# Kernel tuning notes

Hardware: AMD Instinct MI355X
Metric: run time of the kernel (lower is better)

Reference implementation:

```python
import jax, jax.numpy as jnp
import numpy as np
from jax import lax

K = 7            # neighborhood kernel size (odd)
HEADS = 6
DIM = 96
HID = int(DIM * 2.66)   # 255, Restormer-style hidden width


def _ln(x, w, b):
    # WithBias_LayerNorm over the channel axis (to_3d makes C the last dim)
    mu = x.mean(axis=1, keepdims=True)
    var = x.var(axis=1, keepdims=True)  # biased, matches unbiased=False
    return (x - mu) / jnp.sqrt(var + 1e-5) * w[None, :, None, None] + b[None, :, None, None]


def _conv1x1(x, w, b=None):
    y = jnp.einsum('bchw,oc->bohw', x, w)
    return y if b is None else y + b[None, :, None, None]


def _dwconv3x3(x, w, b=None):
    y = lax.conv_general_dilated(x, w, (1, 1), 'SAME',
                                 feature_group_count=x.shape[1],
                                 dimension_numbers=('NCHW', 'OIHW', 'NCHW'))
    return y if b is None else y + b[None, :, None, None]


def _l2norm(x):
    n = jnp.sqrt(jnp.sum(x * x, axis=-1, keepdims=True))
    return x / jnp.maximum(n, 1e-12)  # F.normalize semantics


def _na(x, qkv_w, qkv_b, qkv_dw_w, qkv_dw_b, rpb, temperature, proj_w, proj_b):
    # NeighborhoodAttention with edge-clamped K x K windows and RPB (dilation=1)
    B, C, H, W = x.shape
    hd = C // HEADS
    qkv = _dwconv3x3(_conv1x1(x, qkv_w, qkv_b), qkv_dw_w, qkv_dw_b)      # [B,3C,H,W]
    qkv = qkv.reshape(B, 3, HEADS, hd, H, W).transpose(1, 0, 2, 4, 5, 3)  # [3,B,h,H,W,d]
    q, k, v = _l2norm(qkv[0]), _l2norm(qkv[1]), qkv[2]
    off = K // 2
    ii = jnp.arange(H)
    jj = jnp.arange(W)
    ri = jnp.clip(ii - off, 0, H - K)[:, None] + jnp.arange(K)   # [H,K] neighbor rows
    cj = jnp.clip(jj - off, 0, W - K)[:, None] + jnp.arange(K)   # [W,K] neighbor cols
    bi = ii[:, None] - ri + (K - 1)   # rpb row idx in [0, 2K-2]
    bj = jj[:, None] - cj + (K - 1)
    RI = jnp.repeat(ri.T, K, axis=0)  # [K*K,H]; offset o=ki*K+kj -> ri[:,ki]
    CI = jnp.tile(cj.T, (K, 1))       # [K*K,W]; offset o        -> cj[:,kj]

    def qk_body(_, rc):
        r, c = rc
        kk = k[:, :, r][:, :, :, c]                       # [B,h,H,W,d] gathered keys
        return None, jnp.einsum('bhijd,bhijd->bhij', q, kk)

    _, scores = lax.scan(qk_body, None, (RI, CI))          # [K*K,B,h,H,W]
    attn = jnp.moveaxis(scores, 0, -1)                     # [B,h,H,W,K*K]
    bias = rpb[:, bi][..., bj]                             # [h,H,K,W,K]
    bias = bias.transpose(0, 1, 3, 2, 4).reshape(HEADS, H, W, K * K)
    attn = (attn + bias[None]) * temperature[None, :, None, None, None]
    attn = jax.nn.softmax(attn, axis=-1)

    def av_body(acc, inp):
        r, c, a = inp
        vv = v[:, :, r][:, :, :, c]                        # [B,h,H,W,d] gathered values
        return acc + a[..., None] * vv, None

    out, _ = lax.scan(av_body, jnp.zeros_like(v), (RI, CI, jnp.moveaxis(attn, -1, 0)))
    out = out.transpose(0, 1, 4, 2, 3).reshape(B, C, H, W)
    return _conv1x1(out, proj_w, proj_b)


def _ffn(x, pin_w, dw_w, pout_w):
    y = _dwconv3x3(_conv1x1(x, pin_w), dw_w)               # [B,2*HID,H,W]
    x1, x2 = jnp.split(y, 2, axis=1)
    return _conv1x1(jax.nn.gelu(x1, approximate=False) * x2, pout_w)


def setup_inputs():
    key = jax.random.key(0)
    ks = jax.random.split(key, 18)
    def rn(k, shape, s=0.05):
        return jax.random.normal(k, shape, jnp.float32) * s
    return {
        'x': jax.random.normal(ks[0], (4, DIM, 128, 128), jnp.float32),
        'ln1_w': 1.0 + rn(ks[1], (DIM,), 0.02), 'ln1_b': rn(ks[2], (DIM,), 0.02),
        'qkv_w': rn(ks[3], (3 * DIM, DIM)), 'qkv_b': rn(ks[4], (3 * DIM,), 0.01),
        'qkv_dw_w': rn(ks[5], (3 * DIM, 1, 3, 3)), 'qkv_dw_b': rn(ks[6], (3 * DIM,), 0.01),
        'rpb': rn(ks[7], (HEADS, 2 * K - 1, 2 * K - 1), 0.02),
        'temperature': jnp.ones((HEADS,), jnp.float32),
        'proj_w': rn(ks[8], (DIM, DIM)), 'proj_b': rn(ks[9], (DIM,), 0.01),
        'ln2_w': 1.0 + rn(ks[10], (DIM,), 0.02), 'ln2_b': rn(ks[11], (DIM,), 0.02),
        'pin_w': rn(ks[12], (2 * HID, DIM)),
        'dw_w': rn(ks[13], (2 * HID, 1, 3, 3)),
        'pout_w': rn(ks[14], (DIM, HID)),
        'beta': rn(ks[15], (DIM,), 0.1), 'gamma': rn(ks[16], (DIM,), 0.1),
    }


def reference(x, ln1_w, ln1_b, qkv_w, qkv_b, qkv_dw_w, qkv_dw_b, rpb, temperature,
              proj_w, proj_b, ln2_w, ln2_b, pin_w, dw_w, pout_w, beta, gamma):
    x = x + _na(_ln(x, ln1_w, ln1_b), qkv_w, qkv_b, qkv_dw_w, qkv_dw_b,
                rpb, temperature, proj_w, proj_b) * beta[None, :, None, None]
    x = x + _ffn(_ln(x, ln2_w, ln2_b), pin_w, dw_w, pout_w) * gamma[None, :, None, None]
    return x
```

## Files before the change

### kernel.cpp

```cpp
#include <hip/hip_runtime.h>
#include <math.h>

#define HT   128
#define WD   128
#define HW   16384
#define NB_B 4
#define BHW  65536
#define CD   96
#define C3   288
#define NH   6
#define HD   16
#define HID  255
#define HID2 510
#define KK   7
#define NNB  49

__global__ __launch_bounds__(256) void prep_weights(
    const float* __restrict__ qkv_w, const float* __restrict__ qkv_b,
    const float* __restrict__ ln1_w, const float* __restrict__ ln1_b,
    const float* __restrict__ pin_w, const float* __restrict__ ln2_w,
    const float* __restrict__ ln2_b,
    const float* __restrict__ proj_w, const float* __restrict__ pout_w,
    float* __restrict__ w1t, float* __restrict__ s1, float* __restrict__ b1,
    float* __restrict__ w2t, float* __restrict__ s2, float* __restrict__ b2,
    float* __restrict__ wpt, float* __restrict__ wot)
{
    int o = blockIdx.x * 256 + threadIdx.x;
    if (o < C3) {
        float s = 0.f, bb = qkv_b[o];
        for (int c = 0; c < CD; ++c) {
            float wv = qkv_w[o*CD+c] * ln1_w[c];
            w1t[(size_t)c * C3 + o] = wv;
            s += wv;
            bb += qkv_w[o*CD+c] * ln1_b[c];
        }
        s1[o] = s; b1[o] = bb;
    }
    if (o < HID2) {
        float s = 0.f, bb = 0.f;
        for (int c = 0; c < CD; ++c) {
            float wv = pin_w[o*CD+c] * ln2_w[c];
            w2t[(size_t)c * 512 + o] = wv;
            s += wv;
            bb += pin_w[o*CD+c] * ln2_b[c];
        }
        s2[o] = s; b2[o] = bb;
    } else if (o < 512) {
        for (int c = 0; c < CD; ++c) w2t[(size_t)c * 512 + o] = 0.f;
        s2[o] = 0.f; b2[o] = 0.f;
    }
    if (o < CD) {
        for (int c = 0; c < CD; ++c)
            wpt[(size_t)c * CD + o] = proj_w[o*CD + c];
        for (int c = 0; c < HID; ++c)
            wot[(size_t)c * CD + o] = pout_w[o*HID + c];
    }
}

__global__ __launch_bounds__(256) void ln_stats(
    const float* __restrict__ x, float* __restrict__ mu, float* __restrict__ rsig)
{
    int t  = blockIdx.x * 256 + threadIdx.x;
    int p4 = t * 4;
    int b = p4 >> 14, p = p4 & (HW - 1);
    const float* xp = x + (size_t)b * CD * HW + p;
    float4 s = {0.f,0.f,0.f,0.f}, s2 = {0.f,0.f,0.f,0.f};
    #pragma unroll 4
    for (int c = 0; c < CD; ++c) {
        float4 v = *(const float4*)(xp + (size_t)c * HW);
        s.x += v.x; s.y += v.y; s.z += v.z; s.w += v.w;
        s2.x = fmaf(v.x, v.x, s2.x); s2.y = fmaf(v.y, v.y, s2.y);
        s2.z = fmaf(v.z, v.z, s2.z); s2.w = fmaf(v.w, v.w, s2.w);
    }
    const float inv = 1.f / CD;
    float4 m, r;
    m.x = s.x*inv; m.y = s.y*inv; m.z = s.z*inv; m.w = s.w*inv;
    r.x = rsqrtf(s2.x*inv - m.x*m.x + 1e-5f);
    r.y = rsqrtf(s2.y*inv - m.y*m.y + 1e-5f);
    r.z = rsqrtf(s2.z*inv - m.z*m.z + 1e-5f);
    r.w = rsqrtf(s2.w*inv - m.w*m.w + 1e-5f);
    *(float4*)(mu + p4)   = m;
    *(float4*)(rsig + p4) = r;
}

template<int EPI>
__global__ __launch_bounds__(256) void conv1x1(
    const float* __restrict__ in, const float* __restrict__ wT,
    int Cin, int Cout, int OS,
    const float* __restrict__ S, const float* __restrict__ Bb,
    const float* __restrict__ mu, const float* __restrict__ rsig,
    const float* __restrict__ res, const float* __restrict__ scale,
    float* __restrict__ out)
{
    int t  = blockIdx.y * 256 + threadIdx.x;
    int p4 = t * 4;
    int o0 = blockIdx.x * 16;
    int b = p4 >> 14, p = p4 & (HW - 1);
    const float* ip = in + (size_t)b * Cin * HW + p;
    float4 acc[16];
    #pragma unroll
    for (int u = 0; u < 16; ++u) acc[u] = {0.f,0.f,0.f,0.f};
    #pragma unroll 2
    for (int c = 0; c < Cin; ++c) {
        float4 v = *(const float4*)(ip + (size_t)c * HW);
        const float* wr = wT + (size_t)c * OS + o0;
        #pragma unroll
        for (int u = 0; u < 16; ++u) {
            float wv = wr[u];
            acc[u].x = fmaf(v.x, wv, acc[u].x);
            acc[u].y = fmaf(v.y, wv, acc[u].y);
            acc[u].z = fmaf(v.z, wv, acc[u].z);
            acc[u].w = fmaf(v.w, wv, acc[u].w);
        }
    }
    size_t obase = (size_t)b * Cout * HW + p;
    if (EPI == 0) {
        float4 m = *(const float4*)(mu + p4);
        float4 r = *(const float4*)(rsig + p4);
        #pragma unroll
        for (int u = 0; u < 16; ++u) {
            int o = o0 + u;
            if (o < Cout) {
                float so = S[o], bo = Bb[o];
                float4 ov;
                ov.x = r.x * (acc[u].x - m.x * so) + bo;
                ov.y = r.y * (acc[u].y - m.y * so) + bo;
                ov.z = r.z * (acc[u].z - m.z * so) + bo;
                ov.w = r.w * (acc[u].w - m.w * so) + bo;
                *(float4*)(out + obase + (size_t)o * HW) = ov;
            }
        }
    } else if (EPI == 1) {
        #pragma unroll
        for (int u = 0; u < 16; ++u) {
            int o = o0 + u;
            float bo = Bb[o], sc = scale[o];
            float4 rv = *(const float4*)(res + obase + (size_t)o * HW);
            float4 ov;
            ov.x = rv.x + (acc[u].x + bo) * sc;
            ov.y = rv.y + (acc[u].y + bo) * sc;
            ov.z = rv.z + (acc[u].z + bo) * sc;
            ov.w = rv.w + (acc[u].w + bo) * sc;
            *(float4*)(out + obase + (size_t)o * HW) = ov;
        }
    } else {
        #pragma unroll
        for (int u = 0; u < 16; ++u) {
            int o = o0 + u;
            float sc = scale[o];
            float4 rv = *(const float4*)(res + obase + (size_t)o * HW);
            float4 ov;
            ov.x = rv.x + acc[u].x * sc;
            ov.y = rv.y + acc[u].y * sc;
            ov.z = rv.z + acc[u].z * sc;
            ov.w = rv.w + acc[u].w * sc;
            *(float4*)(out + obase + (size_t)o * HW) = ov;
        }
    }
}

__global__ __launch_bounds__(256) void dwconv3x3(
    const float* __restrict__ in, const float* __restrict__ dwv,
    const float* __restrict__ bias, float* __restrict__ out, int Ch)
{
    int t  = blockIdx.x * 256 + threadIdx.x;
    int p4 = t * 4;
    int bc = blockIdx.y;
    int c  = bc % Ch;
    int h = p4 >> 7, wx = p4 & (WD - 1);
    const float* ip = in + (size_t)bc * HW;
    const float* wk = dwv + c * 9;
    float bz = bias[c];
    float a0 = bz, a1 = bz, a2 = bz, a3 = bz;
    #pragma unroll
    for (int ky = 0; ky < 3; ++ky) {
        int hh = h + ky - 1;
        if (hh < 0 || hh >= HT) continue;
        const float* rowp = ip + hh * WD + wx;
        float vm = (wx > 0)        ? rowp[-1] : 0.f;
        float4 v = *(const float4*)rowp;
        float vp = (wx + 4 < WD)   ? rowp[4]  : 0.f;
        float w0 = wk[ky*3+0], w1 = wk[ky*3+1], w2 = wk[ky*3+2];
        a0 = fmaf(vm,  w0, a0); a0 = fmaf(v.x, w1, a0); a0 = fmaf(v.y, w2, a0);
        a1 = fmaf(v.x, w0, a1); a1 = fmaf(v.y, w1, a1); a1 = fmaf(v.z, w2, a1);
        a2 = fmaf(v.y, w0, a2); a2 = fmaf(v.z, w1, a2); a2 = fmaf(v.w, w2, a2);
        a3 = fmaf(v.z, w0, a3); a3 = fmaf(v.w, w1, a3); a3 = fmaf(vp,  w2, a3);
    }
    float4 ov; ov.x = a0; ov.y = a1; ov.z = a2; ov.w = a3;
    *(float4*)(out + (size_t)bc * HW + p4) = ov;
}

__global__ __launch_bounds__(256) void dw_gate(
    const float* __restrict__ in, const float* __restrict__ dwv,
    float* __restrict__ out)
{
    int t  = blockIdx.x * 256 + threadIdx.x;
    int p4 = t * 4;
    int bj = blockIdx.y;
    int b = bj / HID, j = bj % HID;
    int h = p4 >> 7, wx = p4 & (WD - 1);
    const float* i1 = in + ((size_t)b * HID2 + j) * HW;
    const float* i2 = i1 + (size_t)HID * HW;
    const float* wk1 = dwv + j * 9;
    const float* wk2 = dwv + (j + HID) * 9;
    float a0=0.f,a1=0.f,a2=0.f,a3=0.f, g0=0.f,g1=0.f,g2=0.f,g3=0.f;
    #pragma unroll
    for (int ky = 0; ky < 3; ++ky) {
        int hh = h + ky - 1;
        if (hh < 0 || hh >= HT) continue;
        const float* r1 = i1 + hh * WD + wx;
        const float* r2 = i2 + hh * WD + wx;
        bool lm = (wx > 0), rp = (wx + 4 < WD);
        float um = lm ? r1[-1] : 0.f;
        float4 u = *(const float4*)r1;
        float up = rp ? r1[4] : 0.f;
        float vm = lm ? r2[-1] : 0.f;
        float4 v = *(const float4*)r2;
        float vp = rp ? r2[4] : 0.f;
        float w10 = wk1[ky*3+0], w11 = wk1[ky*3+1], w12 = wk1[ky*3+2];
        float w20 = wk2[ky*3+0], w21 = wk2[ky*3+1], w22 = wk2[ky*3+2];
        a0 = fmaf(um,  w10, a0); a0 = fmaf(u.x, w11, a0); a0 = fmaf(u.y, w12, a0);
        a1 = fmaf(u.x, w10, a1); a1 = fmaf(u.y, w11, a1); a1 = fmaf(u.z, w12, a1);
        a2 = fmaf(u.y, w10, a2); a2 = fmaf(u.z, w11, a2); a2 = fmaf(u.w, w12, a2);
        a3 = fmaf(u.z, w10, a3); a3 = fmaf(u.w, w11, a3); a3 = fmaf(up,  w12, a3);
        g0 = fmaf(vm,  w20, g0); g0 = fmaf(v.x, w21, g0); g0 = fmaf(v.y, w22, g0);
        g1 = fmaf(v.x, w20, g1); g1 = fmaf(v.y, w21, g1); g1 = fmaf(v.z, w22, g1);
        g2 = fmaf(v.y, w20, g2); g2 = fmaf(v.z, w21, g2); g2 = fmaf(v.w, w22, g2);
        g3 = fmaf(v.z, w20, g3); g3 = fmaf(v.w, w21, g3); g3 = fmaf(vp,  w22, g3);
    }
    const float is2 = 0.70710678118654752f;
    float4 ov;
    ov.x = 0.5f * a0 * (1.f + erff(a0 * is2)) * g0;
    ov.y = 0.5f * a1 * (1.f + erff(a1 * is2)) * g1;
    ov.z = 0.5f * a2 * (1.f + erff(a2 * is2)) * g2;
    ov.w = 0.5f * a3 * (1.f + erff(a3 * is2)) * g3;
    *(float4*)(out + ((size_t)b * HID + j) * HW + p4) = ov;
}

__global__ __launch_bounds__(256) void knorm(
    const float* __restrict__ qkv, float* __restrict__ rk)
{
    int t = blockIdx.x * 256 + threadIdx.x;
    int e = t * 4;
    int b = e / (NH * HW);
    int rem = e - b * (NH * HW);
    int h = rem / HW, p = rem & (HW - 1);
    const float* kp = qkv + ((size_t)b * C3 + CD + h * HD) * HW + p;
    float4 s = {0.f,0.f,0.f,0.f};
    #pragma unroll
    for (int d = 0; d < HD; ++d) {
        float4 v = *(const float4*)(kp + (size_t)d * HW);
        s.x = fmaf(v.x, v.x, s.x); s.y = fmaf(v.y, v.y, s.y);
        s.z = fmaf(v.z, v.z, s.z); s.w = fmaf(v.w, v.w, s.w);
    }
    float4 ov;
    ov.x = 1.f / fmaxf(sqrtf(s.x), 1e-12f);
    ov.y = 1.f / fmaxf(sqrtf(s.y), 1e-12f);
    ov.z = 1.f / fmaxf(sqrtf(s.z), 1e-12f);
    ov.w = 1.f / fmaxf(sqrtf(s.w), 1e-12f);
    *(float4*)(rk + e) = ov;
}

__global__ __launch_bounds__(256) void natten(
    const float* __restrict__ qkv, const float* __restrict__ rknorm,
    const float* __restrict__ rpb, const float* __restrict__ temp,
    float* __restrict__ out)
{
    __shared__ float srpb[169];
    int bh = blockIdx.z;
    int b = bh / NH, head = bh % NH;
    if (threadIdx.x < 169) srpb[threadIdx.x] = rpb[head * 169 + threadIdx.x];
    __syncthreads();

    int i = blockIdx.y * 16 + (threadIdx.x >> 4);
    int j = blockIdx.x * 16 + (threadIdx.x & 15);
    const float* qp = qkv + ((size_t)b * C3 + head * HD) * HW + i * WD + j;
    const float* kp = qkv + ((size_t)b * C3 + CD   + head * HD) * HW;
    const float* vp = qkv + ((size_t)b * C3 + 2*CD + head * HD) * HW;
    const float* rkp = rknorm + ((size_t)b * NH + head) * HW;
    float T = temp[head];

    float q[HD]; float qn = 0.f;
    #pragma unroll
    for (int d = 0; d < HD; ++d) { q[d] = qp[(size_t)d * HW]; qn = fmaf(q[d], q[d], qn); }
    qn = 1.f / fmaxf(sqrtf(qn), 1e-12f);
    #pragma unroll
    for (int d = 0; d < HD; ++d) q[d] *= qn;

    int ri0 = min(max(i - 3, 0), HT - KK);
    int cj0 = min(max(j - 3, 0), WD - KK);
    int bi0 = i - ri0 + 6;
    int bj0 = j - cj0 + 6;

    float s[NNB]; float m = -1e30f;
    #pragma unroll
    for (int o = 0; o < NNB; ++o) {
        int r = ri0 + o / KK, c = cj0 + o % KK;
        const float* kk = kp + r * WD + c;
        float dot = 0.f;
        #pragma unroll
        for (int d = 0; d < HD; ++d)
            dot = fmaf(q[d], kk[(size_t)d * HW], dot);
        float sv = (dot * rkp[r * WD + c]
                    + srpb[(bi0 - o / KK) * 13 + (bj0 - o % KK)]) * T;
        s[o] = sv;
        m = fmaxf(m, sv);
    }
    float l = 0.f;
    #pragma unroll
    for (int o = 0; o < NNB; ++o) { float pv = __expf(s[o] - m); s[o] = pv; l += pv; }
    float inv = 1.f / l;
    float ov[HD];
    #pragma unroll
    for (int d = 0; d < HD; ++d) ov[d] = 0.f;
    #pragma unroll
    for (int o = 0; o < NNB; ++o) {
        int r = ri0 + o / KK, c = cj0 + o % KK;
        const float* vv = vp + r * WD + c;
        float pv = s[o];
        #pragma unroll
        for (int d = 0; d < HD; ++d) ov[d] = fmaf(pv, vv[(size_t)d * HW], ov[d]);
    }
    float* op = out + ((size_t)b * CD + head * HD) * HW + i * WD + j;
    #pragma unroll
    for (int d = 0; d < HD; ++d) op[(size_t)d * HW] = ov[d] * inv;
}

extern "C" void kernel_launch(void* const* d_in, const int* in_sizes, int n_in,
                              void* d_out, int out_size, void* d_ws, size_t ws_size,
                              hipStream_t stream)
{
    const float* x        = (const float*)d_in[0];
    const float* ln1_w    = (const float*)d_in[1];
    const float* ln1_b    = (const float*)d_in[2];
    const float* qkv_w    = (const float*)d_in[3];
    const float* qkv_b    = (const float*)d_in[4];
    const float* qkv_dw_w = (const float*)d_in[5];
    const float* qkv_dw_b = (const float*)d_in[6];
    const float* rpb      = (const float*)d_in[7];
    const float* temp     = (const float*)d_in[8];
    const float* proj_w   = (const float*)d_in[9];
    const float* proj_b   = (const float*)d_in[10];
    const float* ln2_w    = (const float*)d_in[11];
    const float* ln2_b    = (const float*)d_in[12];
    const float* pin_w    = (const float*)d_in[13];
    const float* dw_w     = (const float*)d_in[14];
    const float* pout_w   = (const float*)d_in[15];
    const float* beta     = (const float*)d_in[16];
    const float* gamma    = (const float*)d_in[17];
    float* out = (float*)d_out;
    float* f   = (float*)d_ws;
    (void)in_sizes; (void)n_in; (void)out_size; (void)ws_size;

    float* W1T = f;
    float* W2T = W1T + 27648;
    float* WPT = W2T + 49152;
    float* WOT = WPT + 9216;
    float* S1  = WOT + 24480;
    float* B1  = S1 + 512;
    float* S2  = B1 + 512;
    float* B2  = S2 + 512;
    float* MU  = B2 + 512;
    float* RS  = MU + 65536;
    float* R1  = f + 262144;
    float* R2  = R1 + 18874368;
    float* R3  = R2 + 18874368;
    float* R4  = R3 + 16711680;
    float* RK  = R1;

    prep_weights<<<dim3(2), dim3(256), 0, stream>>>(
        qkv_w, qkv_b, ln1_w, ln1_b, pin_w, ln2_w, ln2_b, proj_w, pout_w,
        W1T, S1, B1, W2T, S2, B2, WPT, WOT);
    ln_stats<<<dim3(64), dim3(256), 0, stream>>>(x, MU, RS);
    conv1x1<0><<<dim3(18, 64), dim3(256), 0, stream>>>(
        x, W1T, CD, C3, C3, S1, B1, MU, RS, nullptr, nullptr, R1);
    dwconv3x3<<<dim3(16, NB_B * C3), dim3(256), 0, stream>>>(
        R1, qkv_dw_w, qkv_dw_b, R2, C3);
    knorm<<<dim3(384), dim3(256), 0, stream>>>(R2, RK);
    natten<<<dim3(8, 8, NB_B * NH), dim3(256), 0, stream>>>(R2, RK, rpb, temp, R3);
    conv1x1<1><<<dim3(6, 64), dim3(256), 0, stream>>>(
        R3, WPT, CD, CD, CD, nullptr, proj_b, nullptr, nullptr, x, beta, R4);
    ln_stats<<<dim3(64), dim3(256), 0, stream>>>(R4, MU, RS);
    conv1x1<0><<<dim3(32, 64), dim3(256), 0, stream>>>(
        R4, W2T, CD, HID2, 512, S2, B2, MU, RS, nullptr, nullptr, R1);
    dw_gate<<<dim3(16, NB_B * HID), dim3(256), 0, stream>>>(R1, dw_w, R3);
    conv1x1<2><<<dim3(6, 64), dim3(256), 0, stream>>>(
        R3, WOT, HID, CD, CD, nullptr, nullptr, nullptr, nullptr, R4, gamma, out);
}
```

Measured before the change: 592.0 us.

## Store K and V pixel-major with fused K normalization for neighborhood attention

Splits the depthwise conv into a Q kernel that keeps the channel-planar layout and K/V kernels that write a pixel-major [bh, HW, 16] layout, with K L2-normalized inside the conv. This drops the separate knorm pass. The attention kernel now reads each neighbor's 16-dim key and value as four float4 loads instead of 16 strided scalar loads, and temperature is folded into q and the bias table. The cost is that the K/V conv kernels hold 16 float4 accumulators per thread (more register pressure) and write with a 64-float stride between adjacent threads.

New measurement: 650.8 us. +9.9%, slower.

```diff
diff --git a/kernel.cpp b/kernel.cpp
--- a/kernel.cpp
+++ b/kernel.cpp
@@ -159,16 +159,16 @@
     }
 }
 
-__global__ __launch_bounds__(256) void dwconv3x3(
+__global__ __launch_bounds__(256) void dwconv_q(
     const float* __restrict__ in, const float* __restrict__ dwv,
-    const float* __restrict__ bias, float* __restrict__ out, int Ch)
+    const float* __restrict__ bias, float* __restrict__ out)
 {
     int t  = blockIdx.x * 256 + threadIdx.x;
     int p4 = t * 4;
     int bc = blockIdx.y;
-    int c  = bc % Ch;
+    int b = bc / CD, c = bc % CD;
     int h = p4 >> 7, wx = p4 & (WD - 1);
-    const float* ip = in + (size_t)bc * HW;
+    const float* ip = in + ((size_t)b * C3 + c) * HW;
     const float* wk = dwv + c * 9;
     float bz = bias[c];
     float a0 = bz, a1 = bz, a2 = bz, a3 = bz;
@@ -177,9 +177,9 @@
         int hh = h + ky - 1;
         if (hh < 0 || hh >= HT) continue;
         const float* rowp = ip + hh * WD + wx;
-        float vm = (wx > 0)        ? rowp[-1] : 0.f;
+        float vm = (wx > 0)      ? rowp[-1] : 0.f;
         float4 v = *(const float4*)rowp;
-        float vp = (wx + 4 < WD)   ? rowp[4]  : 0.f;
+        float vp = (wx + 4 < WD) ? rowp[4]  : 0.f;
         float w0 = wk[ky*3+0], w1 = wk[ky*3+1], w2 = wk[ky*3+2];
         a0 = fmaf(vm,  w0, a0); a0 = fmaf(v.x, w1, a0); a0 = fmaf(v.y, w2, a0);
         a1 = fmaf(v.x, w0, a1); a1 = fmaf(v.y, w1, a1); a1 = fmaf(v.z, w2, a1);
@@ -187,7 +187,75 @@
         a3 = fmaf(v.z, w0, a3); a3 = fmaf(v.w, w1, a3); a3 = fmaf(vp,  w2, a3);
     }
     float4 ov; ov.x = a0; ov.y = a1; ov.z = a2; ov.w = a3;
-    *(float4*)(out + (size_t)bc * HW + p4) = ov;
+    *(float4*)(out + ((size_t)b * CD + c) * HW + p4) = ov;
+}
+
+template<bool NORM>
+__global__ __launch_bounds__(256) void dwconv_t(
+    const float* __restrict__ in, const float* __restrict__ dwv,
+    const float* __restrict__ bias, float* __restrict__ outt, int cbase)
+{
+    int t  = blockIdx.x * 256 + threadIdx.x;
+    int p4 = t * 4;
+    int bh = blockIdx.y;
+    int b = bh / NH, head = bh % NH;
+    int h = p4 >> 7, wx = p4 & (WD - 1);
+    float4 acc[16];
+    #pragma unroll
+    for (int hd = 0; hd < 16; ++hd) {
+        int c = cbase + head * HD + hd;
+        const float* ip = in + ((size_t)b * C3 + c) * HW;
+        const float* wk = dwv + c * 9;
+        float bz = bias[c];
+        float a0 = bz, a1 = bz, a2 = bz, a3 = bz;
+        #pragma unroll
+        for (int ky = 0; ky < 3; ++ky) {
+            int hh = h + ky - 1;
+            if (hh < 0 || hh >= HT) continue;
+            const float* rowp = ip + hh * WD + wx;
+            float vm = (wx > 0)      ? rowp[-1] : 0.f;
+            float4 v = *(const float4*)rowp;
+            float vp = (wx + 4 < WD) ? rowp[4]  : 0.f;
+            float w0 = wk[ky*3+0], w1 = wk[ky*3+1], w2 = wk[ky*3+2];
+            a0 = fmaf(vm,  w0, a0); a0 = fmaf(v.x, w1, a0); a0 = fmaf(v.y, w2, a0);
+            a1 = fmaf(v.x, w0, a1); a1 = fmaf(v.y, w1, a1); a1 = fmaf(v.z, w2, a1);
+            a2 = fmaf(v.y, w0, a2); a2 = fmaf(v.z, w1, a2); a2 = fmaf(v.w, w2, a2);
+            a3 = fmaf(v.z, w0, a3); a3 = fmaf(v.w, w1, a3); a3 = fmaf(vp,  w2, a3);
+        }
+        acc[hd] = {a0, a1, a2, a3};
+    }
+    if (NORM) {
+        float n0=0.f, n1=0.f, n2=0.f, n3=0.f;
+        #pragma unroll
+        for (int hd = 0; hd < 16; ++hd) {
+            n0 = fmaf(acc[hd].x, acc[hd].x, n0);
+            n1 = fmaf(acc[hd].y, acc[hd].y, n1);
+            n2 = fmaf(acc[hd].z, acc[hd].z, n2);
+            n3 = fmaf(acc[hd].w, acc[hd].w, n3);
+        }
+        n0 = 1.f / fmaxf(sqrtf(n0), 1e-12f);
+        n1 = 1.f / fmaxf(sqrtf(n1), 1e-12f);
+        n2 = 1.f / fmaxf(sqrtf(n2), 1e-12f);
+        n3 = 1.f / fmaxf(sqrtf(n3), 1e-12f);
+        #pragma unroll
+        for (int hd = 0; hd < 16; ++hd) {
+            acc[hd].x *= n0; acc[hd].y *= n1; acc[hd].z *= n2; acc[hd].w *= n3;
+        }
+    }
+    float* op = outt + ((size_t)bh * HW + p4) * 16;
+#define STORE_PX(pi, comp)                                                    \
+    {                                                                         \
+        float4 w0 = {acc[ 0].comp, acc[ 1].comp, acc[ 2].comp, acc[ 3].comp}; \
+        float4 w1 = {acc[ 4].comp, acc[ 5].comp, acc[ 6].comp, acc[ 7].comp}; \
+        float4 w2 = {acc[ 8].comp, acc[ 9].comp, acc[10].comp, acc[11].comp}; \
+        float4 w3 = {acc[12].comp, acc[13].comp, acc[14].comp, acc[15].comp}; \
+        *(float4*)(op + pi*16 +  0) = w0;                                     \
+        *(float4*)(op + pi*16 +  4) = w1;                                     \
+        *(float4*)(op + pi*16 +  8) = w2;                                     \
+        *(float4*)(op + pi*16 + 12) = w3;                                     \
+    }
+    STORE_PX(0, x) STORE_PX(1, y) STORE_PX(2, z) STORE_PX(3, w)
+#undef STORE_PX
 }
 
 __global__ __launch_bounds__(256) void dw_gate(
@@ -237,53 +305,28 @@
     *(float4*)(out + ((size_t)b * HID + j) * HW + p4) = ov;
 }
 
-__global__ __launch_bounds__(256) void knorm(
-    const float* __restrict__ qkv, float* __restrict__ rk)
-{
-    int t = blockIdx.x * 256 + threadIdx.x;
-    int e = t * 4;
-    int b = e / (NH * HW);
-    int rem = e - b * (NH * HW);
-    int h = rem / HW, p = rem & (HW - 1);
-    const float* kp = qkv + ((size_t)b * C3 + CD + h * HD) * HW + p;
-    float4 s = {0.f,0.f,0.f,0.f};
-    #pragma unroll
-    for (int d = 0; d < HD; ++d) {
-        float4 v = *(const float4*)(kp + (size_t)d * HW);
-        s.x = fmaf(v.x, v.x, s.x); s.y = fmaf(v.y, v.y, s.y);
-        s.z = fmaf(v.z, v.z, s.z); s.w = fmaf(v.w, v.w, s.w);
-    }
-    float4 ov;
-    ov.x = 1.f / fmaxf(sqrtf(s.x), 1e-12f);
-    ov.y = 1.f / fmaxf(sqrtf(s.y), 1e-12f);
-    ov.z = 1.f / fmaxf(sqrtf(s.z), 1e-12f);
-    ov.w = 1.f / fmaxf(sqrtf(s.w), 1e-12f);
-    *(float4*)(rk + e) = ov;
-}
-
 __global__ __launch_bounds__(256) void natten(
-    const float* __restrict__ qkv, const float* __restrict__ rknorm,
-    const float* __restrict__ rpb, const float* __restrict__ temp,
-    float* __restrict__ out)
+    const float* __restrict__ qd, const float* __restrict__ kt,
+    const float* __restrict__ vt, const float* __restrict__ rpb,
+    const float* __restrict__ temp, float* __restrict__ out)
 {
     __shared__ float srpb[169];
     int bh = blockIdx.z;
     int b = bh / NH, head = bh % NH;
-    if (threadIdx.x < 169) srpb[threadIdx.x] = rpb[head * 169 + threadIdx.x];
+    float T = temp[head];
+    if (threadIdx.x < 169) srpb[threadIdx.x] = rpb[head * 169 + threadIdx.x] * T;
     __syncthreads();
 
     int i = blockIdx.y * 16 + (threadIdx.x >> 4);
     int j = blockIdx.x * 16 + (threadIdx.x & 15);
-    const float* qp = qkv + ((size_t)b * C3 + head * HD) * HW + i * WD + j;
-    const float* kp = qkv + ((size_t)b * C3 + CD   + head * HD) * HW;
-    const float* vp = qkv + ((size_t)b * C3 + 2*CD + head * HD) * HW;
-    const float* rkp = rknorm + ((size_t)b * NH + head) * HW;
-    float T = temp[head];
+    const float* qp  = qd + ((size_t)b * CD + head * HD) * HW + i * WD + j;
+    const float* ktb = kt + (size_t)bh * HW * 16;
+    const float* vtb = vt + (size_t)bh * HW * 16;
 
     float q[HD]; float qn = 0.f;
     #pragma unroll
     for (int d = 0; d < HD; ++d) { q[d] = qp[(size_t)d * HW]; qn = fmaf(q[d], q[d], qn); }
-    qn = 1.f / fmaxf(sqrtf(qn), 1e-12f);
+    qn = T / fmaxf(sqrtf(qn), 1e-12f);
     #pragma unroll
     for (int d = 0; d < HD; ++d) q[d] *= qn;
 
@@ -296,13 +339,14 @@
     #pragma unroll
     for (int o = 0; o < NNB; ++o) {
         int r = ri0 + o / KK, c = cj0 + o % KK;
-        const float* kk = kp + r * WD + c;
-        float dot = 0.f;
-        #pragma unroll
-        for (int d = 0; d < HD; ++d)
-            dot = fmaf(q[d], kk[(size_t)d * HW], dot);
-        float sv = (dot * rkp[r * WD + c]
-                    + srpb[(bi0 - o / KK) * 13 + (bj0 - o % KK)]) * T;
+        const float4* kk = (const float4*)(ktb + ((size_t)(r * WD + c)) * 16);
+        float4 k0 = kk[0], k1 = kk[1], k2 = kk[2], k3 = kk[3];
+        float d0 = q[0]*k0.x + q[1]*k0.y + q[2]*k0.z + q[3]*k0.w;
+        float d1 = q[4]*k1.x + q[5]*k1.y + q[6]*k1.z + q[7]*k1.w;
+        float d2 = q[8]*k2.x + q[9]*k2.y + q[10]*k2.z + q[11]*k2.w;
+        float d3 = q[12]*k3.x + q[13]*k3.y + q[14]*k3.z + q[15]*k3.w;
+        float sv = (d0 + d1) + (d2 + d3)
+                 + srpb[(bi0 - o / KK) * 13 + (bj0 - o % KK)];
         s[o] = sv;
         m = fmaxf(m, sv);
     }
@@ -316,10 +360,17 @@
     #pragma unroll
     for (int o = 0; o < NNB; ++o) {
         int r = ri0 + o / KK, c = cj0 + o % KK;
-        const float* vv = vp + r * WD + c;
+        const float4* vv = (const float4*)(vtb + ((size_t)(r * WD + c)) * 16);
+        float4 v0 = vv[0], v1 = vv[1], v2 = vv[2], v3 = vv[3];
         float pv = s[o];
-        #pragma unroll
-        for (int d = 0; d < HD; ++d) ov[d] = fmaf(pv, vv[(size_t)d * HW], ov[d]);
+        ov[0]  = fmaf(pv, v0.x, ov[0]);  ov[1]  = fmaf(pv, v0.y, ov[1]);
+        ov[2]  = fmaf(pv, v0.z, ov[2]);  ov[3]  = fmaf(pv, v0.w, ov[3]);
+        ov[4]  = fmaf(pv, v1.x, ov[4]);  ov[5]  = fmaf(pv, v1.y, ov[5]);
+        ov[6]  = fmaf(pv, v1.z, ov[6]);  ov[7]  = fmaf(pv, v1.w, ov[7]);
+        ov[8]  = fmaf(pv, v2.x, ov[8]);  ov[9]  = fmaf(pv, v2.y, ov[9]);
+        ov[10] = fmaf(pv, v2.z, ov[10]); ov[11] = fmaf(pv, v2.w, ov[11]);
+        ov[12] = fmaf(pv, v3.x, ov[12]); ov[13] = fmaf(pv, v3.y, ov[13]);
+        ov[14] = fmaf(pv, v3.z, ov[14]); ov[15] = fmaf(pv, v3.w, ov[15]);
     }
     float* op = out + ((size_t)b * CD + head * HD) * HW + i * WD + j;
     #pragma unroll
@@ -362,28 +413,34 @@
     float* B2  = S2 + 512;
     float* MU  = B2 + 512;
     float* RS  = MU + 65536;
-    float* R1  = f + 262144;
-    float* R2  = R1 + 18874368;
-    float* R3  = R2 + 18874368;
-    float* R4  = R3 + 16711680;
-    float* RK  = R1;
+    float* A   = f + 262144;
+    float* QKV = A;
+    float* QD  = A + 18874368;
+    float* KT  = QD + 6291456;
+    float* VT  = KT + 6291456;
+    float* AO  = A + 37748736;
+    float* X2  = A + 54460416;
 
     prep_weights<<<dim3(2), dim3(256), 0, stream>>>(
         qkv_w, qkv_b, ln1_w, ln1_b, pin_w, ln2_w, ln2_b, proj_w, pout_w,
         W1T, S1, B1, W2T, S2, B2, WPT, WOT);
     ln_stats<<<dim3(64), dim3(256), 0, stream>>>(x, MU, RS);
     conv1x1<0><<<dim3(18, 64), dim3(256), 0, stream>>>(
-        x, W1T, CD, C3, C3, S1, B1, MU, RS, nullptr, nullptr, R1);
-    dwconv3x3<<<dim3(16, NB_B * C3), dim3(256), 0, stream>>>(
-        R1, qkv_dw_w, qkv_dw_b, R2, C3);
-    knorm<<<dim3(384), dim3(256), 0, stream>>>(R2, RK);
-    natten<<<dim3(8, 8, NB_B * NH), dim3(256), 0, stream>>>(R2, RK, rpb, temp, R3);
+        x, W1T, CD, C3, C3, S1, B1, MU, RS, nullptr, nullptr, QKV);
+    dwconv_q<<<dim3(16, NB_B * CD), dim3(256), 0, stream>>>(
+        QKV, qkv_dw_w, qkv_dw_b, QD);
+    dwconv_t<true><<<dim3(16, NB_B * NH), dim3(256), 0, stream>>>(
+        QKV, qkv_dw_w, qkv_dw_b, KT, CD);
+    dwconv_t<false><<<dim3(16, NB_B * NH), dim3(256), 0, stream>>>(
+        QKV, qkv_dw_w, qkv_dw_b, VT, 2 * CD);
+    natten<<<dim3(8, 8, NB_B * NH), dim3(256), 0, stream>>>(
+        QD, KT, VT, rpb, temp, AO);
     conv1x1<1><<<dim3(6, 64), dim3(256), 0, stream>>>(
-        R3, WPT, CD, CD, CD, nullptr, proj_b, nullptr, nullptr, x, beta, R4);
-    ln_stats<<<dim3(64), dim3(256), 0, stream>>>(R4, MU, RS);
+        AO, WPT, CD, CD, CD, nullptr, proj_b, nullptr, nullptr, x, beta, X2);
+    ln_stats<<<dim3(64), dim3(256), 0, stream>>>(X2, MU, RS);
     conv1x1<0><<<dim3(32, 64), dim3(256), 0, stream>>>(
-        R4, W2T, CD, HID2, 512, S2, B2, MU, RS, nullptr, nullptr, R1);
-    dw_gate<<<dim3(16, NB_B * HID), dim3(256), 0, stream>>>(R1, dw_w, R3);
+        X2, W2T, CD, HID2, 512, S2, B2, MU, RS, nullptr, nullptr, QKV);
+    dw_gate<<<dim3(16, NB_B * HID), dim3(256), 0, stream>>>(QKV, dw_w, AO);
     conv1x1<2><<<dim3(6, 64), dim3(256), 0, stream>>>(
-        R3, WOT, HID, CD, CD, nullptr, nullptr, nullptr, nullptr, R4, gamma, out);
-}
+        AO, WOT, HID, CD, CD, nullptr, nullptr, nullptr, nullptr, X2, gamma, out);
+}
```
